# Optimization experiments

Hardware: AMD Instinct MI355X
Metric: run time of the kernel (lower is better)

## Reference

```python
import jax, jax.numpy as jnp
import numpy as np

N = 50000   # num nodes
E = 500000  # num edges
D = 128     # latent_size


def _mlp_params(key, d_in, d_hid, d_out):
    k1, k2 = jax.random.split(key)
    return (jax.random.normal(k1, (d_in, d_hid), jnp.float32) * 0.05,
            jnp.zeros((d_hid,), jnp.float32),
            jax.random.normal(k2, (d_hid, d_out), jnp.float32) * 0.05,
            jnp.zeros((d_out,), jnp.float32))


def setup_inputs() -> dict:
    key = jax.random.key(0)
    ks = jax.random.split(key, 16)
    inp = {
        'edge_index': jax.random.randint(ks[0], (2, E), 0, N, dtype=jnp.int32),
        'edge_attr': jax.random.randint(ks[1], (E, 1), 0, 3, dtype=jnp.int32) - 1,   # {-1,0,1}; -1 => virtual edge
        'node_type': jax.random.randint(ks[2], (N, 2), 0, 3, dtype=jnp.int32) - 1,  # last col == -1 => global node
        'senders_pos': jax.random.normal(ks[3], (E, 3), jnp.float32),
        'receivers_pos': jax.random.normal(ks[4], (E, 3), jnp.float32),
        'vector_a': jax.random.normal(ks[5], (E, 3), jnp.float32),
        'vector_b': jax.random.normal(ks[6], (E, 3), jnp.float32),
        'vector_c': jax.random.normal(ks[7], (E, 3), jnp.float32),
        'interaction_latent': jax.random.normal(ks[8], (E, D), jnp.float32),
        'w_nodes': jax.random.uniform(ks[9], (N, 1), jnp.float32) + 0.1,  # positive masses
    }
    for name, kk, d_out in (('i1', ks[10], 3), ('i2', ks[11], 3), ('fs', ks[12], 1), ('dx', ks[13], 3)):
        W1, b1, W2, b2 = _mlp_params(kk, D, D, d_out)
        inp[name + '_W1'], inp[name + '_b1'], inp[name + '_W2'], inp[name + '_b2'] = W1, b1, W2, b2
    return inp


def _mlp(x, W1, b1, W2, b2):
    return jax.nn.relu(x @ W1 + b1) @ W2 + b2


def _remove_mean(t, mask, idx):
    # subtract per-node mean of masked edges, only on masked entries
    m = mask[:, None].astype(t.dtype)
    s = jax.ops.segment_sum(t * m, idx, num_segments=N)       # [N,3]
    c = jax.ops.segment_sum(m, idx, num_segments=N)           # [N,1]
    mean = s / jnp.maximum(c, 1.0)
    return t - mean[idx] * m


def reference(edge_index, edge_attr, senders_pos, receivers_pos, vector_a, vector_b,
              vector_c, interaction_latent, w_nodes, node_type,
              i1_W1, i1_b1, i1_W2, i1_b2,
              i2_W1, i2_b1, i2_W2, i2_b2,
              fs_W1, fs_b1, fs_W2, fs_b2,
              dx_W1, dx_b1, dx_W2, dx_b2):
    senders, receivers = edge_index[0], edge_index[1]
    coeff_f = _mlp(interaction_latent, i1_W1, i1_b1, i1_W2, i1_b2)   # [E,3]
    coeff_a = _mlp(interaction_latent, i2_W1, i2_b1, i2_W2, i2_b2)   # [E,3]
    lambda_ij = _mlp(interaction_latent, fs_W1, fs_b1, fs_W2, fs_b2) # [E,1]
    coeff_dx = _mlp(interaction_latent, dx_W1, dx_b1, dx_W2, dx_b2)  # [E,3]

    fij = coeff_f[:, 0:1] * vector_a + coeff_f[:, 1:2] * vector_b + coeff_f[:, 2:3] * vector_c
    aij = coeff_a[:, 0:1] * vector_a + coeff_a[:, 1:2] * vector_b + coeff_a[:, 2:3] * vector_c
    dxij = coeff_dx[:, 0:1] * vector_a + coeff_dx[:, 1:2] * vector_b + coeff_dx[:, 2:3] * vector_c

    is_global = node_type[:, -1] == -1            # [N]
    is_virtual = (edge_attr == -1).reshape(-1)    # [E]

    mask_in = is_virtual & is_global[receivers]
    fij = _remove_mean(fij, mask_in, receivers)
    aij = _remove_mean(aij, mask_in, receivers)
    dxij = _remove_mean(dxij, mask_in, receivers)

    mask_out = is_virtual & is_global[senders]
    fij = _remove_mean(fij, mask_out, senders)
    aij = _remove_mean(aij, mask_out, senders)
    dxij = _remove_mean(dxij, mask_out, senders)

    w_s, w_r = w_nodes[senders], w_nodes[receivers]            # [E,1]
    r0ij = (w_s * senders_pos + w_r * receivers_pos) / (w_s + w_r)
    lever_arm = receivers_pos - r0ij
    torque_contribution = jnp.cross(lever_arm, fij * lambda_ij)
    tauij = aij - torque_contribution
    return (fij, tauij, dxij)
```

## Files before the change

### kernel.cpp

```cpp
#include <hip/hip_runtime.h>
#include <hip/hip_bf16.h>

#define NN 50000
#define NE 500000
#define DD 128

typedef float  f32x4 __attribute__((ext_vector_type(4)));
typedef short  s16x8 __attribute__((ext_vector_type(8)));

struct MlpPtrs { const float* W1; const float* b1; const float* W2; const float* b2; int dout; int obase; };
struct MlpArgs { MlpPtrs m[4]; };

__device__ __forceinline__ unsigned short f2bf(float f) {
    return __builtin_bit_cast(unsigned short, __hip_bfloat16(f));
}

__device__ __forceinline__ float row_reduce16(float v) {
    int x = __builtin_bit_cast(int, v);
    int y;
    float f;
    y = __builtin_amdgcn_update_dpp(0, x, 0x121, 0xf, 0xf, true);
    f = __builtin_bit_cast(float, x) + __builtin_bit_cast(float, y);
    x = __builtin_bit_cast(int, f);
    y = __builtin_amdgcn_update_dpp(0, x, 0x122, 0xf, 0xf, true);
    f = __builtin_bit_cast(float, x) + __builtin_bit_cast(float, y);
    x = __builtin_bit_cast(int, f);
    y = __builtin_amdgcn_update_dpp(0, x, 0x124, 0xf, 0xf, true);
    f = __builtin_bit_cast(float, x) + __builtin_bit_cast(float, y);
    x = __builtin_bit_cast(int, f);
    y = __builtin_amdgcn_update_dpp(0, x, 0x128, 0xf, 0xf, true);
    f = __builtin_bit_cast(float, x) + __builtin_bit_cast(float, y);
    return f;
}

__global__ void prep_w1t_kernel(const float* __restrict__ W1a, const float* __restrict__ W1b,
                                const float* __restrict__ W1c, const float* __restrict__ W1d,
                                unsigned short* __restrict__ w1t)
{
    int idx = blockIdx.x * blockDim.x + threadIdx.x;
    if (idx >= 4 * DD * DD) return;
    int m = idx >> 14, r = idx & 16383;
    int j = r >> 7, k = r & 127;
    const float* W1 = (m == 0) ? W1a : (m == 1) ? W1b : (m == 2) ? W1c : W1d;
    w1t[idx] = f2bf(W1[k * DD + j]);
}

__global__ __launch_bounds__(256) void mlp_mfma_kernel(
    const float* __restrict__ latent, const unsigned short* __restrict__ w1t,
    const float* __restrict__ va, const float* __restrict__ vb, const float* __restrict__ vc,
    const int* __restrict__ receivers, const int* __restrict__ edge_attr,
    const int* __restrict__ node_type,
    float* __restrict__ out, float* __restrict__ lam_ws,
    float* __restrict__ sIn, float* __restrict__ cIn, MlpArgs args)
{
    __shared__ unsigned short Ws[DD * 136];
    __shared__ float W2s[DD * 3];
    __shared__ float Cf[4][32][10];

    const int t = threadIdx.x;
    const int wave = t >> 6, l = t & 63;
    const int lg = l >> 4, lr = l & 15;
    const int e0 = blockIdx.x * 128 + wave * 32;

    s16x8 a[2][4];
    #pragma unroll
    for (int mf = 0; mf < 2; ++mf) {
        int e = e0 + mf * 16 + lr; if (e >= NE) e = NE - 1;
        const float* src = latent + (size_t)e * DD + lg * 8;
        #pragma unroll
        for (int kc = 0; kc < 4; ++kc) {
            float4 x0 = *(const float4*)(src + kc * 32);
            float4 x1 = *(const float4*)(src + kc * 32 + 4);
            s16x8 v;
            v[0] = (short)f2bf(x0.x); v[1] = (short)f2bf(x0.y);
            v[2] = (short)f2bf(x0.z); v[3] = (short)f2bf(x0.w);
            v[4] = (short)f2bf(x1.x); v[5] = (short)f2bf(x1.y);
            v[6] = (short)f2bf(x1.z); v[7] = (short)f2bf(x1.w);
            a[mf][kc] = v;
        }
    }

    for (int m = 0; m < 4; ++m) {
        const MlpPtrs P = args.m[m];
        __syncthreads();
        {
            const uint4* src = (const uint4*)(w1t + m * DD * DD);
            #pragma unroll
            for (int i = 0; i < 8; ++i) {
                int idx16 = t + i * 256;
                uint4 vv = src[idx16];
                int j = idx16 >> 4, k = (idx16 & 15) * 8;
                *(uint4*)&Ws[j * 136 + k] = vv;
            }
        }
        for (int i = t; i < DD * P.dout; i += 256) W2s[i] = P.W2[i];
        __syncthreads();

        f32x4 acc[2][8];
        #pragma unroll
        for (int mf = 0; mf < 2; ++mf)
            #pragma unroll
            for (int nf = 0; nf < 8; ++nf) {
                f32x4 z = {0.f, 0.f, 0.f, 0.f};
                acc[mf][nf] = z;
            }
        #pragma unroll
        for (int nf = 0; nf < 8; ++nf) {
            #pragma unroll
            for (int kc = 0; kc < 4; ++kc) {
                s16x8 b = *(const s16x8*)&Ws[(lr + 16 * nf) * 136 + lg * 8 + kc * 32];
                acc[0][nf] = __builtin_amdgcn_mfma_f32_16x16x32_bf16(a[0][kc], b, acc[0][nf], 0, 0, 0);
                acc[1][nf] = __builtin_amdgcn_mfma_f32_16x16x32_bf16(a[1][kc], b, acc[1][nf], 0, 0, 0);
            }
        }
        #pragma unroll
        for (int nf = 0; nf < 8; ++nf) {
            float bv = P.b1[16 * nf + lr];
            #pragma unroll
            for (int mf = 0; mf < 2; ++mf)
                #pragma unroll
                for (int r = 0; r < 4; ++r)
                    acc[mf][nf][r] = fmaxf(acc[mf][nf][r] + bv, 0.f);
        }
        for (int o = 0; o < P.dout; ++o) {
            float w2v[8];
            #pragma unroll
            for (int nf = 0; nf < 8; ++nf) w2v[nf] = W2s[(16 * nf + lr) * P.dout + o];
            float p[2][4];
            #pragma unroll
            for (int mf = 0; mf < 2; ++mf)
                #pragma unroll
                for (int r = 0; r < 4; ++r) {
                    float s = 0.f;
                    #pragma unroll
                    for (int nf = 0; nf < 8; ++nf) s = fmaf(acc[mf][nf][r], w2v[nf], s);
                    p[mf][r] = row_reduce16(s);
                }
            if (lr == 0) {
                float b2v = P.b2[o];
                #pragma unroll
                for (int mf = 0; mf < 2; ++mf)
                    #pragma unroll
                    for (int r = 0; r < 4; ++r)
                        Cf[wave][mf * 16 + lg * 4 + r][P.obase + o] = p[mf][r] + b2v;
            }
        }
    }
    __syncthreads();

    if (l < 32) {
        const int e = e0 + l;
        if (e < NE) {
            float c[10];
            #pragma unroll
            for (int q = 0; q < 10; ++q) c[q] = Cf[wave][l][q];
            const float ax = va[(size_t)e*3+0], ay = va[(size_t)e*3+1], az = va[(size_t)e*3+2];
            const float bx = vb[(size_t)e*3+0], by = vb[(size_t)e*3+1], bz = vb[(size_t)e*3+2];
            const float cx = vc[(size_t)e*3+0], cy = vc[(size_t)e*3+1], cz = vc[(size_t)e*3+2];
            const size_t o0 = (size_t)e * 3;
            const size_t o1 = (size_t)NE * 3 + o0;
            const size_t o2 = (size_t)2 * NE * 3 + o0;
            const float f0 = c[0]*ax + c[1]*bx + c[2]*cx;
            const float f1 = c[0]*ay + c[1]*by + c[2]*cy;
            const float f2 = c[0]*az + c[1]*bz + c[2]*cz;
            const float a0 = c[3]*ax + c[4]*bx + c[5]*cx;
            const float a1 = c[3]*ay + c[4]*by + c[5]*cy;
            const float a2 = c[3]*az + c[4]*bz + c[5]*cz;
            const float d0 = c[7]*ax + c[8]*bx + c[9]*cx;
            const float d1 = c[7]*ay + c[8]*by + c[9]*cy;
            const float d2 = c[7]*az + c[8]*bz + c[9]*cz;
            out[o0+0] = f0; out[o0+1] = f1; out[o0+2] = f2;
            out[o1+0] = a0; out[o1+1] = a1; out[o1+2] = a2;
            out[o2+0] = d0; out[o2+1] = d1; out[o2+2] = d2;
            lam_ws[e] = c[6];

            if (edge_attr[e] == -1) {
                const int rn = receivers[e];
                if (node_type[2 * rn + 1] == -1) {
                    atomicAdd(&cIn[rn], 1.0f);
                    atomicAdd(&sIn[(size_t)0 * 3 * NN + (size_t)rn * 3 + 0], f0);
                    atomicAdd(&sIn[(size_t)0 * 3 * NN + (size_t)rn * 3 + 1], f1);
                    atomicAdd(&sIn[(size_t)0 * 3 * NN + (size_t)rn * 3 + 2], f2);
                    atomicAdd(&sIn[(size_t)1 * 3 * NN + (size_t)rn * 3 + 0], a0);
                    atomicAdd(&sIn[(size_t)1 * 3 * NN + (size_t)rn * 3 + 1], a1);
                    atomicAdd(&sIn[(size_t)1 * 3 * NN + (size_t)rn * 3 + 2], a2);
                    atomicAdd(&sIn[(size_t)2 * 3 * NN + (size_t)rn * 3 + 0], d0);
                    atomicAdd(&sIn[(size_t)2 * 3 * NN + (size_t)rn * 3 + 1], d1);
                    atomicAdd(&sIn[(size_t)2 * 3 * NN + (size_t)rn * 3 + 2], d2);
                }
            }
        }
    }
}

__global__ void zero_kernel(float* __restrict__ p, int n)
{
    int i = blockIdx.x * blockDim.x + threadIdx.x;
    if (i < n) p[i] = 0.0f;
}

__global__ void apply_r_sum_s_kernel(const int* __restrict__ senders, const int* __restrict__ receivers,
                                     const int* __restrict__ edge_attr, const int* __restrict__ node_type,
                                     float* __restrict__ out,
                                     const float* __restrict__ sIn, const float* __restrict__ cIn,
                                     float* __restrict__ sOut, float* __restrict__ cOut)
{
    int e = blockIdx.x * blockDim.x + threadIdx.x;
    if (e >= NE) return;
    if (edge_attr[e] != -1) return;
    const int r = receivers[e], s = senders[e];
    const bool mr = (node_type[2 * r + 1] == -1);
    const bool ms = (node_type[2 * s + 1] == -1);
    if (!mr && !ms) return;
    float v[9];
    #pragma unroll
    for (int tns = 0; tns < 3; ++tns)
        #pragma unroll
        for (int c2 = 0; c2 < 3; ++c2)
            v[tns * 3 + c2] = out[(size_t)tns * NE * 3 + (size_t)e * 3 + c2];
    if (mr) {
        const float ic = 1.0f / fmaxf(cIn[r], 1.0f);
        #pragma unroll
        for (int tns = 0; tns < 3; ++tns)
            #pragma unroll
            for (int c2 = 0; c2 < 3; ++c2) {
                v[tns * 3 + c2] -= sIn[(size_t)tns * 3 * NN + (size_t)r * 3 + c2] * ic;
                out[(size_t)tns * NE * 3 + (size_t)e * 3 + c2] = v[tns * 3 + c2];
            }
    }
    if (ms) {
        atomicAdd(&cOut[s], 1.0f);
        #pragma unroll
        for (int tns = 0; tns < 3; ++tns)
            #pragma unroll
            for (int c2 = 0; c2 < 3; ++c2)
                atomicAdd(&sOut[(size_t)tns * 3 * NN + (size_t)s * 3 + c2], v[tns * 3 + c2]);
    }
}

__global__ void apply_finalize_kernel(const int* __restrict__ senders, const int* __restrict__ receivers,
                                      const int* __restrict__ edge_attr, const int* __restrict__ node_type,
                                      const float* __restrict__ sp, const float* __restrict__ rp,
                                      const float* __restrict__ wn, const float* __restrict__ lam,
                                      const float* __restrict__ sums, const float* __restrict__ cnt,
                                      float* __restrict__ out)
{
    int e = blockIdx.x * blockDim.x + threadIdx.x;
    if (e >= NE) return;
    const int s = senders[e], r = receivers[e];
    const size_t b = (size_t)e * 3;
    const size_t tb = (size_t)NE * 3 + b;
    const size_t db = (size_t)2 * NE * 3 + b;
    float fx = out[b+0], fy = out[b+1], fz = out[b+2];
    float axx = out[tb+0], ayy = out[tb+1], azz = out[tb+2];
    const bool masked = (edge_attr[e] == -1) && (node_type[2 * s + 1] == -1);
    if (masked) {
        const float ic = 1.0f / fmaxf(cnt[s], 1.0f);
        fx -= sums[(size_t)0 * 3 * NN + (size_t)s * 3 + 0] * ic;
        fy -= sums[(size_t)0 * 3 * NN + (size_t)s * 3 + 1] * ic;
        fz -= sums[(size_t)0 * 3 * NN + (size_t)s * 3 + 2] * ic;
        axx -= sums[(size_t)1 * 3 * NN + (size_t)s * 3 + 0] * ic;
        ayy -= sums[(size_t)1 * 3 * NN + (size_t)s * 3 + 1] * ic;
        azz -= sums[(size_t)1 * 3 * NN + (size_t)s * 3 + 2] * ic;
        out[b+0] = fx; out[b+1] = fy; out[b+2] = fz;
        out[db+0] -= sums[(size_t)2 * 3 * NN + (size_t)s * 3 + 0] * ic;
        out[db+1] -= sums[(size_t)2 * 3 * NN + (size_t)s * 3 + 1] * ic;
        out[db+2] -= sums[(size_t)2 * 3 * NN + (size_t)s * 3 + 2] * ic;
    }
    const float wsv = wn[s], wrv = wn[r];
    const float inv = 1.0f / (wsv + wrv);
    const float spx = sp[b+0], spy = sp[b+1], spz = sp[b+2];
    const float rpx = rp[b+0], rpy = rp[b+1], rpz = rp[b+2];
    const float lx = rpx - (wsv * spx + wrv * rpx) * inv;
    const float ly = rpy - (wsv * spy + wrv * rpy) * inv;
    const float lz = rpz - (wsv * spz + wrv * rpz) * inv;
    const float lv = lam[e];
    const float gx = fx * lv, gy = fy * lv, gz = fz * lv;
    out[tb+0] = axx - (ly * gz - lz * gy);
    out[tb+1] = ayy - (lz * gx - lx * gz);
    out[tb+2] = azz - (lx * gy - ly * gx);
}

extern "C" void kernel_launch(void* const* d_in, const int* in_sizes, int n_in,
                              void* d_out, int out_size, void* d_ws, size_t ws_size,
                              hipStream_t stream)
{
    (void)in_sizes; (void)n_in; (void)out_size; (void)ws_size;

    const int* edge_index    = (const int*)d_in[0];
    const int* edge_attr     = (const int*)d_in[1];
    const int* node_type     = (const int*)d_in[2];
    const float* senders_pos = (const float*)d_in[3];
    const float* recv_pos    = (const float*)d_in[4];
    const float* vector_a    = (const float*)d_in[5];
    const float* vector_b    = (const float*)d_in[6];
    const float* vector_c    = (const float*)d_in[7];
    const float* latent      = (const float*)d_in[8];
    const float* w_nodes     = (const float*)d_in[9];

    MlpArgs ma;
    const int douts[4] = {3, 3, 1, 3};
    const int obase[4] = {0, 3, 6, 7};
    for (int i = 0; i < 4; ++i) {
        ma.m[i].W1 = (const float*)d_in[10 + i * 4 + 0];
        ma.m[i].b1 = (const float*)d_in[10 + i * 4 + 1];
        ma.m[i].W2 = (const float*)d_in[10 + i * 4 + 2];
        ma.m[i].b2 = (const float*)d_in[10 + i * 4 + 3];
        ma.m[i].dout = douts[i];
        ma.m[i].obase = obase[i];
    }

    float* out = (float*)d_out;
    float* lam    = (float*)d_ws;
    float* segbuf = lam + NE;
    float* sIn    = segbuf;
    float* cIn    = sIn + 9 * NN;
    float* sOut   = cIn + NN;
    float* cOut   = sOut + 9 * NN;
    unsigned short* w1t = (unsigned short*)(cOut + NN);

    const int* senders   = edge_index;
    const int* receivers = edge_index + NE;

    hipLaunchKernelGGL(prep_w1t_kernel, dim3((4 * DD * DD + 255) / 256), dim3(256), 0, stream,
                       ma.m[0].W1, ma.m[1].W1, ma.m[2].W1, ma.m[3].W1, w1t);
    hipLaunchKernelGGL(zero_kernel, dim3((20 * NN + 255) / 256), dim3(256), 0, stream,
                       segbuf, 20 * NN);
    hipLaunchKernelGGL(mlp_mfma_kernel, dim3((NE + 127) / 128), dim3(256), 0, stream,
                       latent, w1t, vector_a, vector_b, vector_c,
                       receivers, edge_attr, node_type, out, lam, sIn, cIn, ma);
    dim3 gE((NE + 255) / 256);
    hipLaunchKernelGGL(apply_r_sum_s_kernel, gE, dim3(256), 0, stream, senders, receivers, edge_attr, node_type,
                       out, sIn, cIn, sOut, cOut);
    hipLaunchKernelGGL(apply_finalize_kernel, gE, dim3(256), 0, stream, senders, receivers, edge_attr, node_type,
                       senders_pos, recv_pos, w_nodes, lam, sOut, cOut, out);
}
```

Baseline: 228.8 us.

## Make MLP kernel persistent with all four W1 matrices resident in LDS

The MLP kernel now launches a fixed grid of 256 blocks. Each block loads all four bf16 W1 matrices, the W2 weights and the b1 biases into shared memory once, then loops over edge tiles. This removes the per-tile reload of weights into LDS and the block-level barriers between MLPs. In exchange, about 150KB of LDS per block leaves room for only one 4-wave block per CU, which cuts the latency hiding available for the streaming latent loads and atomics.

```diff
diff --git a/kernel.cpp b/kernel.cpp
--- a/kernel.cpp
+++ b/kernel.cpp
@@ -4,6 +4,7 @@
 #define NN 50000
 #define NE 500000
 #define DD 128
+#define NT ((NE + 127) / 128)
 
 typedef float  f32x4 __attribute__((ext_vector_type(4)));
 typedef short  s16x8 __attribute__((ext_vector_type(8)));
@@ -45,7 +46,7 @@
     w1t[idx] = f2bf(W1[k * DD + j]);
 }
 
-__global__ __launch_bounds__(256) void mlp_mfma_kernel(
+__global__ __launch_bounds__(256) void mlp_persist_kernel(
     const float* __restrict__ latent, const unsigned short* __restrict__ w1t,
     const float* __restrict__ va, const float* __restrict__ vb, const float* __restrict__ vc,
     const int* __restrict__ receivers, const int* __restrict__ edge_attr,
@@ -53,140 +54,148 @@
     float* __restrict__ out, float* __restrict__ lam_ws,
     float* __restrict__ sIn, float* __restrict__ cIn, MlpArgs args)
 {
-    __shared__ unsigned short Ws[DD * 136];
-    __shared__ float W2s[DD * 3];
+    __shared__ unsigned short Ws4[4 * DD * 136];
+    __shared__ float W2s4[4 * DD * 3];
+    __shared__ float B1s4[4 * DD];
     __shared__ float Cf[4][32][10];
 
     const int t = threadIdx.x;
     const int wave = t >> 6, l = t & 63;
     const int lg = l >> 4, lr = l & 15;
-    const int e0 = blockIdx.x * 128 + wave * 32;
-
-    s16x8 a[2][4];
-    #pragma unroll
-    for (int mf = 0; mf < 2; ++mf) {
-        int e = e0 + mf * 16 + lr; if (e >= NE) e = NE - 1;
-        const float* src = latent + (size_t)e * DD + lg * 8;
-        #pragma unroll
-        for (int kc = 0; kc < 4; ++kc) {
-            float4 x0 = *(const float4*)(src + kc * 32);
-            float4 x1 = *(const float4*)(src + kc * 32 + 4);
-            s16x8 v;
-            v[0] = (short)f2bf(x0.x); v[1] = (short)f2bf(x0.y);
-            v[2] = (short)f2bf(x0.z); v[3] = (short)f2bf(x0.w);
-            v[4] = (short)f2bf(x1.x); v[5] = (short)f2bf(x1.y);
-            v[6] = (short)f2bf(x1.z); v[7] = (short)f2bf(x1.w);
-            a[mf][kc] = v;
-        }
-    }
 
     for (int m = 0; m < 4; ++m) {
         const MlpPtrs P = args.m[m];
-        __syncthreads();
-        {
-            const uint4* src = (const uint4*)(w1t + m * DD * DD);
-            #pragma unroll
-            for (int i = 0; i < 8; ++i) {
-                int idx16 = t + i * 256;
-                uint4 vv = src[idx16];
-                int j = idx16 >> 4, k = (idx16 & 15) * 8;
-                *(uint4*)&Ws[j * 136 + k] = vv;
-            }
+        const uint4* src = (const uint4*)(w1t + (size_t)m * DD * DD);
+        #pragma unroll
+        for (int i = 0; i < 8; ++i) {
+            int idx16 = t + i * 256;
+            uint4 vv = src[idx16];
+            int j = idx16 >> 4, k = (idx16 & 15) * 8;
+            *(uint4*)&Ws4[m * DD * 136 + j * 136 + k] = vv;
         }
-        for (int i = t; i < DD * P.dout; i += 256) W2s[i] = P.W2[i];
-        __syncthreads();
-
-        f32x4 acc[2][8];
-        #pragma unroll
-        for (int mf = 0; mf < 2; ++mf)
+        for (int i = t; i < DD * P.dout; i += 256) W2s4[m * DD * 3 + i] = P.W2[i];
+        if (t < DD) B1s4[m * DD + t] = P.b1[t];
+    }
+    __syncthreads();
+
+    for (int tile = blockIdx.x; tile < NT; tile += gridDim.x) {
+        const int e0 = tile * 128 + wave * 32;
+
+        s16x8 a[2][4];
+        #pragma unroll
+        for (int mf = 0; mf < 2; ++mf) {
+            int e = e0 + mf * 16 + lr; if (e >= NE) e = NE - 1;
+            const float* src = latent + (size_t)e * DD + lg * 8;
+            #pragma unroll
+            for (int kc = 0; kc < 4; ++kc) {
+                float4 x0 = *(const float4*)(src + kc * 32);
+                float4 x1 = *(const float4*)(src + kc * 32 + 4);
+                s16x8 v;
+                v[0] = (short)f2bf(x0.x); v[1] = (short)f2bf(x0.y);
+                v[2] = (short)f2bf(x0.z); v[3] = (short)f2bf(x0.w);
+                v[4] = (short)f2bf(x1.x); v[5] = (short)f2bf(x1.y);
+                v[6] = (short)f2bf(x1.z); v[7] = (short)f2bf(x1.w);
+                a[mf][kc] = v;
+            }
+        }
+
+        #pragma unroll
+        for (int m = 0; m < 4; ++m) {
+            const MlpPtrs P = args.m[m];
+            const unsigned short* Wp = &Ws4[m * DD * 136];
+
+            f32x4 acc[2][8];
+            #pragma unroll
+            for (int mf = 0; mf < 2; ++mf)
+                #pragma unroll
+                for (int nf = 0; nf < 8; ++nf) {
+                    f32x4 z = {0.f, 0.f, 0.f, 0.f};
+                    acc[mf][nf] = z;
+                }
             #pragma unroll
             for (int nf = 0; nf < 8; ++nf) {
-                f32x4 z = {0.f, 0.f, 0.f, 0.f};
-                acc[mf][nf] = z;
-            }
-        #pragma unroll
-        for (int nf = 0; nf < 8; ++nf) {
-            #pragma unroll
-            for (int kc = 0; kc < 4; ++kc) {
-                s16x8 b = *(const s16x8*)&Ws[(lr + 16 * nf) * 136 + lg * 8 + kc * 32];
-                acc[0][nf] = __builtin_amdgcn_mfma_f32_16x16x32_bf16(a[0][kc], b, acc[0][nf], 0, 0, 0);
-                acc[1][nf] = __builtin_amdgcn_mfma_f32_16x16x32_bf16(a[1][kc], b, acc[1][nf], 0, 0, 0);
-            }
-        }
-        #pragma unroll
-        for (int nf = 0; nf < 8; ++nf) {
-            float bv = P.b1[16 * nf + lr];
-            #pragma unroll
-            for (int mf = 0; mf < 2; ++mf)
-                #pragma unroll
-                for (int r = 0; r < 4; ++r)
-                    acc[mf][nf][r] = fmaxf(acc[mf][nf][r] + bv, 0.f);
-        }
-        for (int o = 0; o < P.dout; ++o) {
-            float w2v[8];
-            #pragma unroll
-            for (int nf = 0; nf < 8; ++nf) w2v[nf] = W2s[(16 * nf + lr) * P.dout + o];
-            float p[2][4];
-            #pragma unroll
-            for (int mf = 0; mf < 2; ++mf)
-                #pragma unroll
-                for (int r = 0; r < 4; ++r) {
-                    float s = 0.f;
-                    #pragma unroll
-                    for (int nf = 0; nf < 8; ++nf) s = fmaf(acc[mf][nf][r], w2v[nf], s);
-                    p[mf][r] = row_reduce16(s);
+                #pragma unroll
+                for (int kc = 0; kc < 4; ++kc) {
+                    s16x8 b = *(const s16x8*)&Wp[(lr + 16 * nf) * 136 + lg * 8 + kc * 32];
+                    acc[0][nf] = __builtin_amdgcn_mfma_f32_16x16x32_bf16(a[0][kc], b, acc[0][nf], 0, 0, 0);
+                    acc[1][nf] = __builtin_amdgcn_mfma_f32_16x16x32_bf16(a[1][kc], b, acc[1][nf], 0, 0, 0);
                 }
-            if (lr == 0) {
-                float b2v = P.b2[o];
+            }
+            #pragma unroll
+            for (int nf = 0; nf < 8; ++nf) {
+                float bv = B1s4[m * DD + 16 * nf + lr];
                 #pragma unroll
                 for (int mf = 0; mf < 2; ++mf)
                     #pragma unroll
                     for (int r = 0; r < 4; ++r)
-                        Cf[wave][mf * 16 + lg * 4 + r][P.obase + o] = p[mf][r] + b2v;
+                        acc[mf][nf][r] = fmaxf(acc[mf][nf][r] + bv, 0.f);
+            }
+            for (int o = 0; o < P.dout; ++o) {
+                float w2v[8];
+                #pragma unroll
+                for (int nf = 0; nf < 8; ++nf)
+                    w2v[nf] = W2s4[m * DD * 3 + (16 * nf + lr) * P.dout + o];
+                float p[2][4];
+                #pragma unroll
+                for (int mf = 0; mf < 2; ++mf)
+                    #pragma unroll
+                    for (int r = 0; r < 4; ++r) {
+                        float s = 0.f;
+                        #pragma unroll
+                        for (int nf = 0; nf < 8; ++nf) s = fmaf(acc[mf][nf][r], w2v[nf], s);
+                        p[mf][r] = row_reduce16(s);
+                    }
+                if (lr == 0) {
+                    float b2v = P.b2[o];
+                    #pragma unroll
+                    for (int mf = 0; mf < 2; ++mf)
+                        #pragma unroll
+                        for (int r = 0; r < 4; ++r)
+                            Cf[wave][mf * 16 + lg * 4 + r][P.obase + o] = p[mf][r] + b2v;
+                }
             }
         }
-    }
-    __syncthreads();
-
-    if (l < 32) {
-        const int e = e0 + l;
-        if (e < NE) {
-            float c[10];
-            #pragma unroll
-            for (int q = 0; q < 10; ++q) c[q] = Cf[wave][l][q];
-            const float ax = va[(size_t)e*3+0], ay = va[(size_t)e*3+1], az = va[(size_t)e*3+2];
-            const float bx = vb[(size_t)e*3+0], by = vb[(size_t)e*3+1], bz = vb[(size_t)e*3+2];
-            const float cx = vc[(size_t)e*3+0], cy = vc[(size_t)e*3+1], cz = vc[(size_t)e*3+2];
-            const size_t o0 = (size_t)e * 3;
-            const size_t o1 = (size_t)NE * 3 + o0;
-            const size_t o2 = (size_t)2 * NE * 3 + o0;
-            const float f0 = c[0]*ax + c[1]*bx + c[2]*cx;
-            const float f1 = c[0]*ay + c[1]*by + c[2]*cy;
-            const float f2 = c[0]*az + c[1]*bz + c[2]*cz;
-            const float a0 = c[3]*ax + c[4]*bx + c[5]*cx;
-            const float a1 = c[3]*ay + c[4]*by + c[5]*cy;
-            const float a2 = c[3]*az + c[4]*bz + c[5]*cz;
-            const float d0 = c[7]*ax + c[8]*bx + c[9]*cx;
-            const float d1 = c[7]*ay + c[8]*by + c[9]*cy;
-            const float d2 = c[7]*az + c[8]*bz + c[9]*cz;
-            out[o0+0] = f0; out[o0+1] = f1; out[o0+2] = f2;
-            out[o1+0] = a0; out[o1+1] = a1; out[o1+2] = a2;
-            out[o2+0] = d0; out[o2+1] = d1; out[o2+2] = d2;
-            lam_ws[e] = c[6];
-
-            if (edge_attr[e] == -1) {
-                const int rn = receivers[e];
-                if (node_type[2 * rn + 1] == -1) {
-                    atomicAdd(&cIn[rn], 1.0f);
-                    atomicAdd(&sIn[(size_t)0 * 3 * NN + (size_t)rn * 3 + 0], f0);
-                    atomicAdd(&sIn[(size_t)0 * 3 * NN + (size_t)rn * 3 + 1], f1);
-                    atomicAdd(&sIn[(size_t)0 * 3 * NN + (size_t)rn * 3 + 2], f2);
-                    atomicAdd(&sIn[(size_t)1 * 3 * NN + (size_t)rn * 3 + 0], a0);
-                    atomicAdd(&sIn[(size_t)1 * 3 * NN + (size_t)rn * 3 + 1], a1);
-                    atomicAdd(&sIn[(size_t)1 * 3 * NN + (size_t)rn * 3 + 2], a2);
-                    atomicAdd(&sIn[(size_t)2 * 3 * NN + (size_t)rn * 3 + 0], d0);
-                    atomicAdd(&sIn[(size_t)2 * 3 * NN + (size_t)rn * 3 + 1], d1);
-                    atomicAdd(&sIn[(size_t)2 * 3 * NN + (size_t)rn * 3 + 2], d2);
+
+        if (l < 32) {
+            const int e = e0 + l;
+            if (e < NE) {
+                float c[10];
+                #pragma unroll
+                for (int q = 0; q < 10; ++q) c[q] = Cf[wave][l][q];
+                const float ax = va[(size_t)e*3+0], ay = va[(size_t)e*3+1], az = va[(size_t)e*3+2];
+                const float bx = vb[(size_t)e*3+0], by = vb[(size_t)e*3+1], bz = vb[(size_t)e*3+2];
+                const float cx = vc[(size_t)e*3+0], cy = vc[(size_t)e*3+1], cz = vc[(size_t)e*3+2];
+                const size_t o0 = (size_t)e * 3;
+                const size_t o1 = (size_t)NE * 3 + o0;
+                const size_t o2 = (size_t)2 * NE * 3 + o0;
+                const float f0 = c[0]*ax + c[1]*bx + c[2]*cx;
+                const float f1 = c[0]*ay + c[1]*by + c[2]*cy;
+                const float f2 = c[0]*az + c[1]*bz + c[2]*cz;
+                const float a0 = c[3]*ax + c[4]*bx + c[5]*cx;
+                const float a1 = c[3]*ay + c[4]*by + c[5]*cy;
+                const float a2 = c[3]*az + c[4]*bz + c[5]*cz;
+                const float d0 = c[7]*ax + c[8]*bx + c[9]*cx;
+                const float d1 = c[7]*ay + c[8]*by + c[9]*cy;
+                const float d2 = c[7]*az + c[8]*bz + c[9]*cz;
+                out[o0+0] = f0; out[o0+1] = f1; out[o0+2] = f2;
+                out[o1+0] = a0; out[o1+1] = a1; out[o1+2] = a2;
+                out[o2+0] = d0; out[o2+1] = d1; out[o2+2] = d2;
+                lam_ws[e] = c[6];
+
+                if (edge_attr[e] == -1) {
+                    const int rn = receivers[e];
+                    if (node_type[2 * rn + 1] == -1) {
+                        atomicAdd(&cIn[rn], 1.0f);
+                        atomicAdd(&sIn[(size_t)0 * 3 * NN + (size_t)rn * 3 + 0], f0);
+                        atomicAdd(&sIn[(size_t)0 * 3 * NN + (size_t)rn * 3 + 1], f1);
+                        atomicAdd(&sIn[(size_t)0 * 3 * NN + (size_t)rn * 3 + 2], f2);
+                        atomicAdd(&sIn[(size_t)1 * 3 * NN + (size_t)rn * 3 + 0], a0);
+                        atomicAdd(&sIn[(size_t)1 * 3 * NN + (size_t)rn * 3 + 1], a1);
+                        atomicAdd(&sIn[(size_t)1 * 3 * NN + (size_t)rn * 3 + 2], a2);
+                        atomicAdd(&sIn[(size_t)2 * 3 * NN + (size_t)rn * 3 + 0], d0);
+                        atomicAdd(&sIn[(size_t)2 * 3 * NN + (size_t)rn * 3 + 1], d1);
+                        atomicAdd(&sIn[(size_t)2 * 3 * NN + (size_t)rn * 3 + 2], d2);
+                    }
                 }
             }
         }
@@ -326,7 +335,7 @@
                        ma.m[0].W1, ma.m[1].W1, ma.m[2].W1, ma.m[3].W1, w1t);
     hipLaunchKernelGGL(zero_kernel, dim3((20 * NN + 255) / 256), dim3(256), 0, stream,
                        segbuf, 20 * NN);
-    hipLaunchKernelGGL(mlp_mfma_kernel, dim3((NE + 127) / 128), dim3(256), 0, stream,
+    hipLaunchKernelGGL(mlp_persist_kernel, dim3(256), dim3(256), 0, stream,
                        latent, w1t, vector_a, vector_b, vector_c,
                        receivers, edge_attr, node_type, out, lam, sIn, cIn, ma);
     dim3 gE((NE + 255) / 256);
```

Result: slower. 589.1 us (+157.5%).
